# Performance work log

Measured on AMD Instinct MI355X. Metric: run time of the kernel, lower is better.

## Reference

```python
import jax, jax.numpy as jnp
import numpy as np

H = 64  # hidden size (matched to ~22K params per the module docstring)


def _lstm_cell(h, c, x, W_ih, W_hh, b):
    # PyTorch gate order: i, f, g, o. x: [B, in], h/c: [B, H]
    gates = x @ W_ih.T + h @ W_hh.T + b            # [B, 4H]
    i, f, g, o = jnp.split(gates, 4, axis=-1)
    i = jax.nn.sigmoid(i)
    f = jax.nn.sigmoid(f)
    g = jnp.tanh(g)
    o = jax.nn.sigmoid(o)
    c_new = f * c + i * g
    h_new = o * jnp.tanh(c_new)
    return h_new, c_new


def setup_inputs() -> dict:
    key = jax.random.key(0)
    ks = jax.random.split(key, 12)
    B, T = 2048, 512
    k = 1.0 / np.sqrt(H)  # PyTorch LSTM/Linear init bound
    u = lambda kk, shape: jax.random.uniform(kk, shape, jnp.float32, -k, k)
    return {
        "context": jax.random.normal(ks[0], (B, T), jnp.float32),
        "W_ih_enc": u(ks[1], (4 * H, 1)),
        "W_hh_enc": u(ks[2], (4 * H, H)),
        "b_ih_enc": u(ks[3], (4 * H,)),
        "b_hh_enc": u(ks[4], (4 * H,)),
        "W_ih_dec": u(ks[5], (4 * H, 1)),
        "W_hh_dec": u(ks[6], (4 * H, H)),
        "b_ih_dec": u(ks[7], (4 * H,)),
        "b_hh_dec": u(ks[8], (4 * H,)),
        "W_head": u(ks[9], (1, H)),
        "b_head": u(ks[10], (1,)),
        "n_steps": 256,
    }


def reference(context, W_ih_enc, W_hh_enc, b_ih_enc, b_hh_enc,
              W_ih_dec, W_hh_dec, b_ih_dec, b_hh_dec,
              W_head, b_head, n_steps):
    B = context.shape[0]
    dt = context.dtype
    b_enc = b_ih_enc + b_hh_enc
    b_dec = b_ih_dec + b_hh_dec

    # --- encode context step-by-step (batch_first LSTM over T) ---
    def enc_step(carry, x_t):  # x_t: [B]
        h, c = carry
        h, c = _lstm_cell(h, c, x_t[:, None], W_ih_enc, W_hh_enc, b_enc)
        return (h, c), None

    h0 = jnp.zeros((B, H), dt)
    c0 = jnp.zeros((B, H), dt)
    (h, c), _ = jax.lax.scan(enc_step, (h0, c0), context.T)  # scan over T

    z0 = context[:, -1:]  # [B, 1] last context value

    def dec_step(carry, _):
        h_d, c_d, z = carry
        h_d, c_d = _lstm_cell(h_d, c_d, z, W_ih_dec, W_hh_dec, b_dec)
        z_next = h_d @ W_head.T + b_head  # [B, 1]
        return (h_d, c_d, z_next), z_next[:, 0]

    _, preds = jax.lax.scan(dec_step, (h, c, z0), None, length=n_steps)  # [n_steps, B]
    return preds.T  # [B, n_steps]
```

## Files before the change

### kernel.cpp

```cpp
#include <hip/hip_runtime.h>
#include <cstddef>
#include <cstdint>

#define TMAX 512
#define HDIM 64

typedef _Float16 half2v __attribute__((ext_vector_type(2)));

__device__ __forceinline__ float fsig(float x) {
    x = fminf(fmaxf(x, -30.f), 30.f);
    float e = __expf(-x);
    return __builtin_amdgcn_rcpf(1.f + e);
}
__device__ __forceinline__ float ftanh(float x) {
    x = fminf(fmaxf(x, -15.f), 15.f);
    float e = __expf(2.f * x);
    return (e - 1.f) * __builtin_amdgcn_rcpf(e + 1.f);
}

#if __has_builtin(__builtin_amdgcn_fdot2)
__device__ __forceinline__ float dot2acc(half2v a, half2v b, float c) {
    return __builtin_amdgcn_fdot2(a, b, c, false);
}
#else
__device__ __forceinline__ float dot2acc(half2v a, half2v b, float c) {
    return fmaf((float)a.y, (float)b.y, fmaf((float)a.x, (float)b.x, c));
}
#endif

__global__ __launch_bounds__(64, 2)
void lstm_wave_kernel(const float* __restrict__ ctx_g,
                      const float* __restrict__ Wih_e,
                      const float* __restrict__ Whh_e,
                      const float* __restrict__ bih_e,
                      const float* __restrict__ bhh_e,
                      const float* __restrict__ Wih_d,
                      const float* __restrict__ Whh_d,
                      const float* __restrict__ bih_d,
                      const float* __restrict__ bhh_d,
                      const float* __restrict__ Whead,
                      const float* __restrict__ bhead,
                      float* __restrict__ out,
                      int T, int n_steps)
{
    __shared__ __align__(16) float    ctx_s[TMAX];
    __shared__ __align__(16) _Float16 h_s[HDIM];

    const int lane = threadIdx.x;
    const int row  = blockIdx.x;

    const float* ctxr = ctx_g + (size_t)row * T;
    for (int t = lane; t < T; t += 64) ctx_s[t] = ctxr[t];

    half2v w2[4][32];
    float  wih[4], bias[4];
    #pragma unroll
    for (int g = 0; g < 4; ++g) {
        const int j = lane + (g << 6);
        const float2* wr = reinterpret_cast<const float2*>(Whh_e + (size_t)j * HDIM);
        #pragma unroll
        for (int k = 0; k < 32; ++k) {
            float2 wv = wr[k];
            w2[g][k] = half2v{(_Float16)wv.x, (_Float16)wv.y};
        }
        wih[g]  = Wih_e[j];
        bias[g] = bih_e[j] + bhh_e[j];
    }

    float c = 0.f, h = 0.f;
    h_s[lane] = (_Float16)0.f;

    for (int t = 0; t < T; ++t) {
        const float x = ctx_s[t];
        float a0 = fmaf(x, wih[0], bias[0]);
        float a1 = fmaf(x, wih[1], bias[1]);
        float a2 = fmaf(x, wih[2], bias[2]);
        float a3 = fmaf(x, wih[3], bias[3]);
        #pragma unroll
        for (int ch = 0; ch < 8; ++ch) {
            half2v hp[4];
            *reinterpret_cast<uint4*>(hp) =
                reinterpret_cast<const uint4*>(h_s)[ch];
            #pragma unroll
            for (int e = 0; e < 4; ++e) {
                const int k = ch * 4 + e;
                a0 = dot2acc(w2[0][k], hp[e], a0);
                a1 = dot2acc(w2[1][k], hp[e], a1);
                a2 = dot2acc(w2[2][k], hp[e], a2);
                a3 = dot2acc(w2[3][k], hp[e], a3);
            }
        }
        const float ig = fsig(a0);
        const float fg = fsig(a1);
        const float gg = ftanh(a2);
        const float og = fsig(a3);
        c = fmaf(fg, c, ig * gg);
        h = og * ftanh(c);
        h_s[lane] = (_Float16)h;
    }

    #pragma unroll
    for (int g = 0; g < 4; ++g) {
        const int j = lane + (g << 6);
        const float2* wr = reinterpret_cast<const float2*>(Whh_d + (size_t)j * HDIM);
        #pragma unroll
        for (int k = 0; k < 32; ++k) {
            float2 wv = wr[k];
            w2[g][k] = half2v{(_Float16)wv.x, (_Float16)wv.y};
        }
        wih[g]  = Wih_d[j];
        bias[g] = bih_d[j] + bhh_d[j];
    }
    const float wh = Whead[lane];
    const float bh = bhead[0];
    float z = ctx_s[T - 1];

    for (int s = 0; s < n_steps; ++s) {
        float a0 = fmaf(z, wih[0], bias[0]);
        float a1 = fmaf(z, wih[1], bias[1]);
        float a2 = fmaf(z, wih[2], bias[2]);
        float a3 = fmaf(z, wih[3], bias[3]);
        #pragma unroll
        for (int ch = 0; ch < 8; ++ch) {
            half2v hp[4];
            *reinterpret_cast<uint4*>(hp) =
                reinterpret_cast<const uint4*>(h_s)[ch];
            #pragma unroll
            for (int e = 0; e < 4; ++e) {
                const int k = ch * 4 + e;
                a0 = dot2acc(w2[0][k], hp[e], a0);
                a1 = dot2acc(w2[1][k], hp[e], a1);
                a2 = dot2acc(w2[2][k], hp[e], a2);
                a3 = dot2acc(w2[3][k], hp[e], a3);
            }
        }
        const float ig = fsig(a0);
        const float fg = fsig(a1);
        const float gg = ftanh(a2);
        const float og = fsig(a3);
        c = fmaf(fg, c, ig * gg);
        h = og * ftanh(c);
        h_s[lane] = (_Float16)h;

        float p = h * wh;
        #pragma unroll
        for (int off = 32; off >= 1; off >>= 1)
            p += __shfl_xor(p, off);
        z = p + bh;
        if (lane == 0) out[(size_t)row * n_steps + s] = z;
    }
}

extern "C" void kernel_launch(void* const* d_in, const int* in_sizes, int n_in,
                              void* d_out, int out_size, void* d_ws, size_t ws_size,
                              hipStream_t stream)
{
    const float* ctx   = (const float*)d_in[0];
    const float* Wih_e = (const float*)d_in[1];
    const float* Whh_e = (const float*)d_in[2];
    const float* bih_e = (const float*)d_in[3];
    const float* bhh_e = (const float*)d_in[4];
    const float* Wih_d = (const float*)d_in[5];
    const float* Whh_d = (const float*)d_in[6];
    const float* bih_d = (const float*)d_in[7];
    const float* bhh_d = (const float*)d_in[8];
    const float* Whead = (const float*)d_in[9];
    const float* bhead = (const float*)d_in[10];
    float* out = (float*)d_out;

    const int B = 2048;
    const int T = in_sizes[0] / B;
    const int n_steps = out_size / B;

    lstm_wave_kernel<<<dim3(B), dim3(64), 0, stream>>>(
        ctx, Wih_e, Whh_e, bih_e, bhh_e,
        Wih_d, Whh_d, bih_d, bhh_d,
        Whead, bhead, out, T, n_steps);
}
```

Measured before the change: 600.3 us.

## Batch 8 rows per block and compute LSTM gate matmul with MFMA

Replaces the one-wave-per-row dot2 recurrence with 512-thread blocks that each handle 8 batch rows. Each step's h·W_hh product runs as 16x16x32 f16 MFMA tiles, with the 8 waves splitting the 256 gate columns. Gate activations are written to LDS and reassembled per row, using a unified sigmoid/tanh helper. This cuts the scalar FMA work per step, at the cost of two block-wide barriers per timestep and padding half of the MFMA rows.

```diff
diff --git a/kernel.cpp b/kernel.cpp
--- a/kernel.cpp
+++ b/kernel.cpp
@@ -1,35 +1,21 @@
 #include <hip/hip_runtime.h>
+#include <cstdint>
 #include <cstddef>
-#include <cstdint>
 
-#define TMAX 512
-#define HDIM 64
+#define RPB    8
+#define TMAX   512
+#define HPITCH 72
 
-typedef _Float16 half2v __attribute__((ext_vector_type(2)));
+typedef _Float16 f16x8 __attribute__((ext_vector_type(8)));
+typedef float    f32x4 __attribute__((ext_vector_type(4)));
 
-__device__ __forceinline__ float fsig(float x) {
-    x = fminf(fmaxf(x, -30.f), 30.f);
-    float e = __expf(-x);
-    return __builtin_amdgcn_rcpf(1.f + e);
-}
-__device__ __forceinline__ float ftanh(float x) {
-    x = fminf(fmaxf(x, -15.f), 15.f);
-    float e = __expf(2.f * x);
-    return (e - 1.f) * __builtin_amdgcn_rcpf(e + 1.f);
+__device__ __forceinline__ float act_gate(float s, float m1, float pa, float pb) {
+    float e = __expf(s * m1);
+    return fmaf(__builtin_amdgcn_rcpf(1.f + e), pa, pb);
 }
 
-#if __has_builtin(__builtin_amdgcn_fdot2)
-__device__ __forceinline__ float dot2acc(half2v a, half2v b, float c) {
-    return __builtin_amdgcn_fdot2(a, b, c, false);
-}
-#else
-__device__ __forceinline__ float dot2acc(half2v a, half2v b, float c) {
-    return fmaf((float)a.y, (float)b.y, fmaf((float)a.x, (float)b.x, c));
-}
-#endif
-
-__global__ __launch_bounds__(64, 2)
-void lstm_wave_kernel(const float* __restrict__ ctx_g,
+__global__ __launch_bounds__(512, 2)
+void lstm_mfma_kernel(const float* __restrict__ ctx_g,
                       const float* __restrict__ Wih_e,
                       const float* __restrict__ Whh_e,
                       const float* __restrict__ bih_e,
@@ -43,111 +29,122 @@
                       float* __restrict__ out,
                       int T, int n_steps)
 {
-    __shared__ __align__(16) float    ctx_s[TMAX];
-    __shared__ __align__(16) _Float16 h_s[HDIM];
+    __shared__ __align__(16) float    ctx_s[RPB][TMAX];
+    __shared__ __align__(16) float    gates_s[RPB][256];
+    __shared__ __align__(16) _Float16 h_s[16][HPITCH];
+    __shared__ float z_s[RPB];
 
-    const int lane = threadIdx.x;
-    const int row  = blockIdx.x;
+    const int tid  = threadIdx.x;
+    const int lane = tid & 63;
+    const int w    = tid >> 6;
+    const int b0   = blockIdx.x * RPB;
+    const int c16  = lane & 15;
+    const int g4   = lane >> 4;
+    const int gate = lane & 3;
+    const int rbase = (g4 & 1) * 4;
 
-    const float* ctxr = ctx_g + (size_t)row * T;
-    for (int t = lane; t < T; t += 64) ctx_s[t] = ctxr[t];
+    for (int i = tid; i < RPB * T; i += 512) {
+        int r = i / T, t = i - r * T;
+        ctx_s[r][t] = ctx_g[(size_t)(b0 + r) * T + t];
+    }
+    for (int i = tid; i < 16 * HPITCH; i += 512)
+        reinterpret_cast<_Float16*>(h_s)[i] = (_Float16)0;
 
-    half2v w2[4][32];
-    float  wih[4], bias[4];
-    #pragma unroll
-    for (int g = 0; g < 4; ++g) {
-        const int j = lane + (g << 6);
-        const float2* wr = reinterpret_cast<const float2*>(Whh_e + (size_t)j * HDIM);
-        #pragma unroll
-        for (int k = 0; k < 32; ++k) {
-            float2 wv = wr[k];
-            w2[g][k] = half2v{(_Float16)wv.x, (_Float16)wv.y};
+    const float m1 = (gate == 2) ? -2.f : -1.f;
+    const float pa = (gate == 2) ?  2.f :  1.f;
+    const float pb = (gate == 2) ? -1.f :  0.f;
+
+    f16x8 b00, b01, b10, b11;
+    float wih0, wih1, bias0, bias1;
+
+    auto load_consts = [&](const float* Whh, const float* Wih,
+                           const float* bih, const float* bhh) {
+        const int cp0 = 32 * w + c16;
+        const int cp1 = cp0 + 16;
+        const int j0  = ((cp0 & 3) << 6) | (cp0 >> 2);
+        const int j1  = ((cp1 & 3) << 6) | (cp1 >> 2);
+        wih0 = Wih[j0];  bias0 = bih[j0] + bhh[j0];
+        wih1 = Wih[j1];  bias1 = bih[j1] + bhh[j1];
+        const float* p;
+        f16x8 bb;
+        #pragma unroll 1
+        for (int q = 0; q < 4; ++q) {
+            const int j  = (q >> 1) ? j1 : j0;
+            const int kt = q & 1;
+            p = Whh + j * 64 + kt * 32 + g4 * 8;
+            #pragma unroll
+            for (int e = 0; e < 8; ++e) bb[e] = (_Float16)p[e];
+            if (q == 0) b00 = bb; else if (q == 1) b01 = bb;
+            else if (q == 2) b10 = bb; else b11 = bb;
         }
-        wih[g]  = Wih_e[j];
-        bias[g] = bih_e[j] + bhh_e[j];
+    };
+
+    load_consts(Whh_e, Wih_e, bih_e, bhh_e);
+    const float wh = Whead[lane];
+    const float bh = bhead[0];
+
+    float c = 0.f;
+    __syncthreads();
+
+    auto do_step = [&](float x0, float x1, float x2, float x3) -> float {
+        f16x8 a0 = *reinterpret_cast<const f16x8*>(&h_s[c16][g4 * 8]);
+        f16x8 a1 = *reinterpret_cast<const f16x8*>(&h_s[c16][32 + g4 * 8]);
+        f32x4 acc0, acc1;
+        acc0[0] = fmaf(x0, wih0, bias0); acc0[1] = fmaf(x1, wih0, bias0);
+        acc0[2] = fmaf(x2, wih0, bias0); acc0[3] = fmaf(x3, wih0, bias0);
+        acc1[0] = fmaf(x0, wih1, bias1); acc1[1] = fmaf(x1, wih1, bias1);
+        acc1[2] = fmaf(x2, wih1, bias1); acc1[3] = fmaf(x3, wih1, bias1);
+        acc0 = __builtin_amdgcn_mfma_f32_16x16x32_f16(a0, b00, acc0, 0, 0, 0);
+        acc0 = __builtin_amdgcn_mfma_f32_16x16x32_f16(a1, b01, acc0, 0, 0, 0);
+        acc1 = __builtin_amdgcn_mfma_f32_16x16x32_f16(a0, b10, acc1, 0, 0, 0);
+        acc1 = __builtin_amdgcn_mfma_f32_16x16x32_f16(a1, b11, acc1, 0, 0, 0);
+        if (g4 < 2) {
+            const int col0 = 32 * w + c16;
+            #pragma unroll
+            for (int reg = 0; reg < 4; ++reg) {
+                gates_s[rbase + reg][col0]      = act_gate(acc0[reg], m1, pa, pb);
+                gates_s[rbase + reg][col0 + 16] = act_gate(acc1[reg], m1, pa, pb);
+            }
+        }
+        __syncthreads();
+        float4 gv = *reinterpret_cast<const float4*>(&gates_s[w][lane * 4]);
+        c = fmaf(gv.y, c, gv.x * gv.z);
+        float e2 = __expf(-2.f * c);
+        float th = fmaf(__builtin_amdgcn_rcpf(1.f + e2), 2.f, -1.f);
+        float h  = gv.w * th;
+        h_s[w][lane] = (_Float16)h;
+        return h;
+    };
+
+    for (int t = 0; t < T; ++t) {
+        float x0 = ctx_s[rbase + 0][t];
+        float x1 = ctx_s[rbase + 1][t];
+        float x2 = ctx_s[rbase + 2][t];
+        float x3 = ctx_s[rbase + 3][t];
+        do_step(x0, x1, x2, x3);
+        __syncthreads();
     }
 
-    float c = 0.f, h = 0.f;
-    h_s[lane] = (_Float16)0.f;
-
-    for (int t = 0; t < T; ++t) {
-        const float x = ctx_s[t];
-        float a0 = fmaf(x, wih[0], bias[0]);
-        float a1 = fmaf(x, wih[1], bias[1]);
-        float a2 = fmaf(x, wih[2], bias[2]);
-        float a3 = fmaf(x, wih[3], bias[3]);
-        #pragma unroll
-        for (int ch = 0; ch < 8; ++ch) {
-            half2v hp[4];
-            *reinterpret_cast<uint4*>(hp) =
-                reinterpret_cast<const uint4*>(h_s)[ch];
-            #pragma unroll
-            for (int e = 0; e < 4; ++e) {
-                const int k = ch * 4 + e;
-                a0 = dot2acc(w2[0][k], hp[e], a0);
-                a1 = dot2acc(w2[1][k], hp[e], a1);
-                a2 = dot2acc(w2[2][k], hp[e], a2);
-                a3 = dot2acc(w2[3][k], hp[e], a3);
-            }
-        }
-        const float ig = fsig(a0);
-        const float fg = fsig(a1);
-        const float gg = ftanh(a2);
-        const float og = fsig(a3);
-        c = fmaf(fg, c, ig * gg);
-        h = og * ftanh(c);
-        h_s[lane] = (_Float16)h;
-    }
-
-    #pragma unroll
-    for (int g = 0; g < 4; ++g) {
-        const int j = lane + (g << 6);
-        const float2* wr = reinterpret_cast<const float2*>(Whh_d + (size_t)j * HDIM);
-        #pragma unroll
-        for (int k = 0; k < 32; ++k) {
-            float2 wv = wr[k];
-            w2[g][k] = half2v{(_Float16)wv.x, (_Float16)wv.y};
-        }
-        wih[g]  = Wih_d[j];
-        bias[g] = bih_d[j] + bhh_d[j];
-    }
-    const float wh = Whead[lane];
-    const float bh = bhead[0];
-    float z = ctx_s[T - 1];
+    if (tid < RPB) z_s[tid] = ctx_s[tid][T - 1];
+    load_consts(Whh_d, Wih_d, bih_d, bhh_d);
+    __syncthreads();
 
     for (int s = 0; s < n_steps; ++s) {
-        float a0 = fmaf(z, wih[0], bias[0]);
-        float a1 = fmaf(z, wih[1], bias[1]);
-        float a2 = fmaf(z, wih[2], bias[2]);
-        float a3 = fmaf(z, wih[3], bias[3]);
-        #pragma unroll
-        for (int ch = 0; ch < 8; ++ch) {
-            half2v hp[4];
-            *reinterpret_cast<uint4*>(hp) =
-                reinterpret_cast<const uint4*>(h_s)[ch];
-            #pragma unroll
-            for (int e = 0; e < 4; ++e) {
-                const int k = ch * 4 + e;
-                a0 = dot2acc(w2[0][k], hp[e], a0);
-                a1 = dot2acc(w2[1][k], hp[e], a1);
-                a2 = dot2acc(w2[2][k], hp[e], a2);
-                a3 = dot2acc(w2[3][k], hp[e], a3);
-            }
-        }
-        const float ig = fsig(a0);
-        const float fg = fsig(a1);
-        const float gg = ftanh(a2);
-        const float og = fsig(a3);
-        c = fmaf(fg, c, ig * gg);
-        h = og * ftanh(c);
-        h_s[lane] = (_Float16)h;
-
+        float x0 = z_s[rbase + 0];
+        float x1 = z_s[rbase + 1];
+        float x2 = z_s[rbase + 2];
+        float x3 = z_s[rbase + 3];
+        float h = do_step(x0, x1, x2, x3);
         float p = h * wh;
         #pragma unroll
         for (int off = 32; off >= 1; off >>= 1)
             p += __shfl_xor(p, off);
-        z = p + bh;
-        if (lane == 0) out[(size_t)row * n_steps + s] = z;
+        if (lane == 0) {
+            const float zn = p + bh;
+            z_s[w] = zn;
+            out[(size_t)(b0 + w) * n_steps + s] = zn;
+        }
+        __syncthreads();
     }
 }
 
@@ -172,7 +169,7 @@
     const int T = in_sizes[0] / B;
     const int n_steps = out_size / B;
 
-    lstm_wave_kernel<<<dim3(B), dim3(64), 0, stream>>>(
+    lstm_mfma_kernel<<<dim3(B / RPB), dim3(512), 0, stream>>>(
         ctx, Wih_e, Whh_e, bih_e, bhh_e,
         Wih_d, Whh_d, bih_d, bhh_d,
         Whead, bhead, out, T, n_steps);
```

After: 1.065 ms. 77.4% more time.
